# Optimization experiments

Hardware: AMD Instinct MI355X
Metric: run time of the kernel (lower is better)

The kernel has to match this reference:

```python
import jax, jax.numpy as jnp
import numpy as np

N = 100000        # nodes
E = 3200000       # edges (avg degree 32)
B = 64            # graphs in the batch
IN_DIM = 128
HEADS = 4
C1 = 8            # conv1 out_channels per head
C2 = 4            # conv2 out_channels per head
OUT_DIM = 10
EPS = 1e-16       # PyG softmax denominator eps


def _lin(key, fan_in, fan_out):
    return jax.random.normal(key, (fan_in, fan_out), jnp.float32) / np.sqrt(fan_in)


def setup_inputs() -> dict:
    key = jax.random.key(0)
    ks = jax.random.split(key, 16)
    x = jax.random.normal(ks[0], (N, IN_DIM), jnp.float32)
    edge_index = jax.random.randint(ks[1], (2, E), 0, N)
    batch = jnp.sort(jax.random.randint(ks[2], (N,), 0, B))
    d1 = HEADS * C1  # 32
    d2 = HEADS * C2  # 16
    inp = {
        "x": x, "edge_index": edge_index, "batch": batch,
        # conv1 (TransformerConv in=128 -> heads*8 = 32)
        "Wq1": _lin(ks[3], IN_DIM, d1), "bq1": jnp.zeros((d1,), jnp.float32),
        "Wk1": _lin(ks[4], IN_DIM, d1), "bk1": jnp.zeros((d1,), jnp.float32),
        "Wv1": _lin(ks[5], IN_DIM, d1), "bv1": jnp.zeros((d1,), jnp.float32),
        "Ws1": _lin(ks[6], IN_DIM, d1), "bs1": jnp.zeros((d1,), jnp.float32),
        # conv2 (in=32 -> heads*4 = 16)
        "Wq2": _lin(ks[7], d1, d2), "bq2": jnp.zeros((d2,), jnp.float32),
        "Wk2": _lin(ks[8], d1, d2), "bk2": jnp.zeros((d2,), jnp.float32),
        "Wv2": _lin(ks[9], d1, d2), "bv2": jnp.zeros((d2,), jnp.float32),
        "Ws2": _lin(ks[10], d1, d2), "bs2": jnp.zeros((d2,), jnp.float32),
        # fc (16 -> 10)
        "Wfc": _lin(ks[11], d2, OUT_DIM), "bfc": jnp.zeros((OUT_DIM,), jnp.float32),
    }
    return inp


def transformer_conv(x, src, dst, Wq, bq, Wk, bk, Wv, bv, Ws, bs, heads):
    n = x.shape[0]
    hc = Wq.shape[1]
    c = hc // heads
    q = (x @ Wq + bq).reshape(n, heads, c)
    k = (x @ Wk + bk).reshape(n, heads, c)
    v = (x @ Wv + bv).reshape(n, heads, c)
    # edge-wise attention logits: query at dst, key at src -> [E, H]
    alpha = jnp.einsum('ehc,ehc->eh', q[dst], k[src]) / np.sqrt(c).astype(np.float32)
    # segment softmax over incoming edges of each dst node
    amax = jax.ops.segment_max(alpha, dst, num_segments=n)           # [N,H]
    ea = jnp.exp(alpha - amax[dst])
    denom = jax.ops.segment_sum(ea, dst, num_segments=n)             # [N,H]
    w = ea / (denom[dst] + EPS)                                      # [E,H]
    msg = v[src] * w[:, :, None]                                     # [E,H,C]
    out = jax.ops.segment_sum(msg, dst, num_segments=n).reshape(n, hc)
    return out + x @ Ws + bs  # root/skip connection


def reference(x, edge_index, batch,
              Wq1, bq1, Wk1, bk1, Wv1, bv1, Ws1, bs1,
              Wq2, bq2, Wk2, bk2, Wv2, bv2, Ws2, bs2,
              Wfc, bfc):
    src, dst = edge_index[0], edge_index[1]
    h = transformer_conv(x, src, dst, Wq1, bq1, Wk1, bk1, Wv1, bv1, Ws1, bs1, HEADS)
    h = jax.nn.relu(h)
    h = transformer_conv(h, src, dst, Wq2, bq2, Wk2, bk2, Wv2, bv2, Ws2, bs2, HEADS)
    h = jax.nn.relu(h)
    # global mean pool per graph
    sums = jax.ops.segment_sum(h, batch, num_segments=B)             # [B,16]
    cnt = jax.ops.segment_sum(jnp.ones((h.shape[0],), h.dtype), batch, num_segments=B)
    pooled = sums / jnp.maximum(cnt, 1.0)[:, None]
    return pooled @ Wfc + bfc                                        # [B,OUT_DIM]
```

## Files before the change

kernel.cpp:

```cpp
#include <hip/hip_runtime.h>

#define HEADS 4
#define EPS 1e-16f
#define NR 256
#define EPB 2048
#define DCH 2048

typedef float floatx2 __attribute__((ext_vector_type(2)));

__device__ inline int rangeOf(int dst, int rdiv, float rinv) {
    int q = (int)((float)dst * rinv);
    if (q > NR - 1) q = NR - 1;
    if ((long long)q * rdiv > dst) --q;
    else if ((long long)(q + 1) * rdiv <= dst) ++q;
    return q;
}

__global__ __launch_bounds__(256) void scatter_count(
    const int* __restrict__ ei, int E, int rdiv, float rinv,
    int* __restrict__ pcnt)
{
    __shared__ int cnt[NR];
    int b = blockIdx.x, t = threadIdx.x;
    int b0 = b * EPB;
    int nloc = min(EPB, E - b0);
    cnt[t] = 0;
    __syncthreads();
    #pragma unroll
    for (int u = 0; u < 8; ++u) {
        int li = u * 256 + t;
        if (li < nloc)
            atomicAdd(&cnt[rangeOf(ei[E + b0 + li], rdiv, rinv)], 1);
    }
    __syncthreads();
    pcnt[(size_t)b * NR + t] = cnt[t];
}

__global__ __launch_bounds__(256) void qprefix(
    int* __restrict__ pcnt, int nb, int* __restrict__ qtot)
{
    __shared__ int part[256];
    int q = blockIdx.x, t = threadIdx.x;
    int per = (nb + 255) >> 8;
    int lo = t * per, hi = min(lo + per, nb);
    int s = 0;
    for (int b = lo; b < hi; ++b) s += pcnt[(size_t)b * NR + q];
    part[t] = s;
    __syncthreads();
    for (int off = 1; off < 256; off <<= 1) {
        int a = (t >= off) ? part[t - off] : 0;
        __syncthreads();
        part[t] += a;
        __syncthreads();
    }
    if (t == 255) qtot[q] = part[255];
    int pre = (t == 0) ? 0 : part[t - 1];
    for (int b = lo; b < hi; ++b) {
        int c = pcnt[(size_t)b * NR + q];
        pcnt[(size_t)b * NR + q] = pre;
        pre += c;
    }
}

__global__ void qscan(const int* __restrict__ qtot, int* __restrict__ rstart)
{
    __shared__ int tmp[NR];
    int t = threadIdx.x;
    tmp[t] = qtot[t];
    __syncthreads();
    for (int off = 1; off < NR; off <<= 1) {
        int a = (t >= off) ? tmp[t - off] : 0;
        __syncthreads();
        tmp[t] += a;
        __syncthreads();
    }
    rstart[t] = (t == 0) ? 0 : tmp[t - 1];
    if (t == NR - 1) rstart[NR] = tmp[NR - 1];
}

__global__ __launch_bounds__(256) void scatter_place(
    const int* __restrict__ ei, int E, int rdiv, float rinv,
    const int* __restrict__ pcnt, const int* __restrict__ rstart,
    int* __restrict__ rsrc, int* __restrict__ rdst)
{
    __shared__ int2 lrec[EPB];
    __shared__ unsigned char lq[EPB];
    __shared__ int cnt[NR], base[NR], scn[NR];
    int b = blockIdx.x, t = threadIdx.x;
    int b0 = b * EPB;
    int nloc = min(EPB, E - b0);
    cnt[t] = 0;
    __syncthreads();
    int myq[8], myoff[8];
    int2 myrec[8];
    #pragma unroll
    for (int u = 0; u < 8; ++u) {
        int li = u * 256 + t;
        if (li < nloc) {
            int e = b0 + li;
            int sv = ei[e], dv = ei[E + e];
            int q = rangeOf(dv, rdiv, rinv);
            myq[u] = q;
            myrec[u] = make_int2(sv, dv);
            myoff[u] = atomicAdd(&cnt[q], 1);
        } else myq[u] = -1;
    }
    __syncthreads();
    scn[t] = cnt[t];
    __syncthreads();
    for (int off = 1; off < 256; off <<= 1) {
        int a = (t >= off) ? scn[t - off] : 0;
        __syncthreads();
        scn[t] += a;
        __syncthreads();
    }
    base[t] = (t == 0) ? 0 : scn[t - 1];
    __syncthreads();
    #pragma unroll
    for (int u = 0; u < 8; ++u) {
        if (myq[u] >= 0) {
            int slot = base[myq[u]] + myoff[u];
            lrec[slot] = myrec[u];
            lq[slot] = (unsigned char)myq[u];
        }
    }
    __syncthreads();
    #pragma unroll
    for (int u = 0; u < 8; ++u) {
        int s2 = u * 256 + t;
        if (s2 < nloc) {
            int q = lq[s2];
            int g = rstart[q] + pcnt[(size_t)b * NR + q] + (s2 - base[q]);
            int2 r = lrec[s2];
            rsrc[g] = r.x;
            rdst[g] = r.y;
        }
    }
}

__global__ __launch_bounds__(256) void deg_range(
    const int* __restrict__ rdst, const int* __restrict__ rstart,
    int* __restrict__ deg, int* __restrict__ row_ptr, int n, int rdiv, int E)
{
    __shared__ int h[512];
    __shared__ int psum[256];
    int q = blockIdx.x, t = threadIdx.x;
    int lo = q * rdiv, hi = min(lo + rdiv, n);
    int nn = hi - lo;
    if (nn <= 0) {
        if (t == 0 && q == NR - 1) row_ptr[n] = E;
        return;
    }
    for (int i = t; i < 512; i += 256) h[i] = 0;
    __syncthreads();
    int rlo = rstart[q], rhi = rstart[q + 1];
    for (int i = rlo + t; i < rhi; i += 256)
        atomicAdd(&h[rdst[i] - lo], 1);
    __syncthreads();
    int s0 = h[2 * t], s1 = h[2 * t + 1];
    psum[t] = s0 + s1;
    __syncthreads();
    for (int off = 1; off < 256; off <<= 1) {
        int a = (t >= off) ? psum[t - off] : 0;
        __syncthreads();
        psum[t] += a;
        __syncthreads();
    }
    int base = rlo + ((t == 0) ? 0 : psum[t - 1]);
    if (2 * t < nn)     { row_ptr[lo + 2 * t] = base;          deg[lo + 2 * t] = s0; }
    if (2 * t + 1 < nn) { row_ptr[lo + 2 * t + 1] = base + s0; deg[lo + 2 * t + 1] = s1; }
    if (t == 0 && q == NR - 1) row_ptr[n] = E;
}

__global__ __launch_bounds__(256) void place_range(
    const int* __restrict__ rsrc, const int* __restrict__ rdst,
    const int* __restrict__ rstart, const int* __restrict__ row_ptr,
    int* __restrict__ col, int n, int rdiv)
{
    __shared__ int cur[512];
    int q = blockIdx.x;
    int lo = q * rdiv, hi = min(lo + rdiv, n);
    int nn = hi - lo;
    if (nn <= 0) return;
    for (int i = threadIdx.x; i < nn; i += 256) cur[i] = row_ptr[lo + i];
    __syncthreads();
    int rlo = rstart[q], rhi = rstart[q + 1];
    for (int i = rlo + threadIdx.x; i < rhi; i += 256) {
        int pos = atomicAdd(&cur[rdst[i] - lo], 1);
        col[pos] = rsrc[i];
    }
}

__global__ __launch_bounds__(256) void dsort_count(
    const int* __restrict__ deg, int* __restrict__ phd, int n)
{
    __shared__ int h[256];
    int t = threadIdx.x;
    h[t] = 0;
    __syncthreads();
    int lo = blockIdx.x * DCH, hi = min(lo + DCH, n);
    for (int i = lo + t; i < hi; i += 256)
        atomicAdd(&h[min(deg[i], 255)], 1);
    __syncthreads();
    phd[blockIdx.x * 256 + t] = h[t];
}

__global__ __launch_bounds__(256) void dsort_prefix(
    int* __restrict__ phd, int nbd)
{
    __shared__ int tot[256];
    int t = threadIdx.x;
    int s = 0;
    for (int b = 0; b < nbd; ++b) s += phd[b * 256 + t];
    tot[t] = s;
    __syncthreads();
    for (int off = 1; off < 256; off <<= 1) {
        int a = (t >= off) ? tot[t - off] : 0;
        __syncthreads();
        tot[t] += a;
        __syncthreads();
    }
    int running = (t == 0) ? 0 : tot[t - 1];
    for (int b = 0; b < nbd; ++b) {
        int c = phd[b * 256 + t];
        phd[b * 256 + t] = running;
        running += c;
    }
}

__global__ __launch_bounds__(256) void dsort_place(
    const int* __restrict__ deg, const int* __restrict__ phd,
    int* __restrict__ order, int n)
{
    __shared__ int lcur[256];
    int t = threadIdx.x;
    lcur[t] = phd[blockIdx.x * 256 + t];
    __syncthreads();
    int lo = blockIdx.x * DCH, hi = min(lo + DCH, n);
    for (int i = lo + t; i < hi; i += 256) {
        int pos = atomicAdd(&lcur[min(deg[i], 255)], 1);
        order[pos] = i;
    }
}

__global__ __launch_bounds__(256) void proj1_kernel(
    const float* __restrict__ x,
    const float* __restrict__ Wq, const float* __restrict__ bq,
    const float* __restrict__ Wk, const float* __restrict__ bk,
    const float* __restrict__ Wv, const float* __restrict__ bv,
    const float* __restrict__ Ws, const float* __restrict__ bs,
    float* __restrict__ qs1, unsigned char* __restrict__ kv1, int n)
{
    __shared__ float Wl[128][128];
    __shared__ float xl[32][128];
    for (int i = threadIdx.x; i < 128 * 128; i += 256) {
        int k = i >> 7, c = i & 127;
        int sub = c >> 5, j = c & 31;
        const float* W = (sub == 0) ? Wq : (sub == 1) ? Wk : (sub == 2) ? Wv : Ws;
        Wl[k][c] = W[k * 32 + j];
    }
    int col4 = (threadIdx.x & 31) * 4;
    int sub = col4 >> 5, j = col4 & 31;
    float4 bias4;
    {
        const float* b = (sub == 0) ? bq : (sub == 1) ? bk : (sub == 2) ? bv : bs;
        bias4 = *(const float4*)(b + j);
    }
    int rb = (threadIdx.x >> 5) * 4;
    __syncthreads();
    for (int row0 = blockIdx.x * 32; row0 < n; row0 += gridDim.x * 32) {
        #pragma unroll
        for (int u = 0; u < 4; ++u) {
            int i = threadIdx.x + u * 256;
            int r = i >> 5, c4 = (i & 31) * 4;
            int gr = row0 + r;
            float4 xv = (gr < n) ? *(const float4*)(x + (size_t)gr * 128 + c4)
                                 : make_float4(0.f, 0.f, 0.f, 0.f);
            *(float4*)(&xl[r][c4]) = xv;
        }
        __syncthreads();
        float4 a0 = bias4, a1 = bias4, a2 = bias4, a3 = bias4;
        #pragma unroll 4
        for (int k = 0; k < 128; k += 4) {
            float4 xv0 = *(const float4*)(&xl[rb + 0][k]);
            float4 xv1 = *(const float4*)(&xl[rb + 1][k]);
            float4 xv2 = *(const float4*)(&xl[rb + 2][k]);
            float4 xv3 = *(const float4*)(&xl[rb + 3][k]);
            float4 w0 = *(const float4*)(&Wl[k + 0][col4]);
            float4 w1 = *(const float4*)(&Wl[k + 1][col4]);
            float4 w2 = *(const float4*)(&Wl[k + 2][col4]);
            float4 w3 = *(const float4*)(&Wl[k + 3][col4]);
            a0.x += xv0.x*w0.x + xv0.y*w1.x + xv0.z*w2.x + xv0.w*w3.x;
            a0.y += xv0.x*w0.y + xv0.y*w1.y + xv0.z*w2.y + xv0.w*w3.y;
            a0.z += xv0.x*w0.z + xv0.y*w1.z + xv0.z*w2.z + xv0.w*w3.z;
            a0.w += xv0.x*w0.w + xv0.y*w1.w + xv0.z*w2.w + xv0.w*w3.w;
            a1.x += xv1.x*w0.x + xv1.y*w1.x + xv1.z*w2.x + xv1.w*w3.x;
            a1.y += xv1.x*w0.y + xv1.y*w1.y + xv1.z*w2.y + xv1.w*w3.y;
            a1.z += xv1.x*w0.z + xv1.y*w1.z + xv1.z*w2.z + xv1.w*w3.z;
            a1.w += xv1.x*w0.w + xv1.y*w1.w + xv1.z*w2.w + xv1.w*w3.w;
            a2.x += xv2.x*w0.x + xv2.y*w1.x + xv2.z*w2.x + xv2.w*w3.x;
            a2.y += xv2.x*w0.y + xv2.y*w1.y + xv2.z*w2.y + xv2.w*w3.y;
            a2.z += xv2.x*w0.z + xv2.y*w1.z + xv2.z*w2.z + xv2.w*w3.z;
            a2.w += xv2.x*w0.w + xv2.y*w1.w + xv2.z*w2.w + xv2.w*w3.w;
            a3.x += xv3.x*w0.x + xv3.y*w1.x + xv3.z*w2.x + xv3.w*w3.x;
            a3.y += xv3.x*w0.y + xv3.y*w1.y + xv3.z*w2.y + xv3.w*w3.y;
            a3.z += xv3.x*w0.z + xv3.y*w1.z + xv3.z*w2.z + xv3.w*w3.z;
            a3.w += xv3.x*w0.w + xv3.y*w1.w + xv3.z*w2.w + xv3.w*w3.w;
        }
        #pragma unroll
        for (int r = 0; r < 4; ++r) {
            int row = row0 + rb + r;
            if (row < n) {
                float4 acc = (r == 0) ? a0 : (r == 1) ? a1 : (r == 2) ? a2 : a3;
                if (sub == 0)
                    *(float4*)(qs1 + (size_t)row * 64 + j) = acc;
                else if (sub == 3)
                    *(float4*)(qs1 + (size_t)row * 64 + 32 + j) = acc;
                else {
                    unsigned u8 = __builtin_amdgcn_cvt_pk_fp8_f32(acc.x, acc.y, 0u, false);
                    u8 = __builtin_amdgcn_cvt_pk_fp8_f32(acc.z, acc.w, u8, true);
                    *(unsigned*)(kv1 + (size_t)row * 64 + ((sub == 1) ? 0 : 32) + j) = u8;
                }
            }
        }
        __syncthreads();
    }
}

__global__ __launch_bounds__(256) void proj2_kernel(
    const float* __restrict__ h1,
    const float* __restrict__ Wq, const float* __restrict__ bq,
    const float* __restrict__ Wk, const float* __restrict__ bk,
    const float* __restrict__ Wv, const float* __restrict__ bv,
    const float* __restrict__ Ws, const float* __restrict__ bs,
    float* __restrict__ qs2, unsigned char* __restrict__ kv2, int n)
{
    __shared__ float Wl[32][64];
    __shared__ float bl[64];
    __shared__ float xl[4][32];
    for (int i = threadIdx.x; i < 32 * 64; i += 256) {
        int k = i >> 6, c = i & 63;
        int sub = c >> 4, j = c & 15;
        const float* W = (sub == 0) ? Wq : (sub == 1) ? Wk : (sub == 2) ? Wv : Ws;
        Wl[k][c] = W[k * 16 + j];
    }
    if (threadIdx.x < 64) {
        int c = threadIdx.x, sub = c >> 4, j = c & 15;
        const float* b = (sub == 0) ? bq : (sub == 1) ? bk : (sub == 2) ? bv : bs;
        bl[c] = b[j];
    }
    __syncthreads();
    int r = threadIdx.x >> 6, col = threadIdx.x & 63;
    int sub = col >> 4, j = col & 15;
    for (int row0 = blockIdx.x * 4; row0 < n; row0 += gridDim.x * 4) {
        int li = threadIdx.x;
        if (li < 128) {
            int rr = row0 + (li >> 5);
            if (rr < n) xl[li >> 5][li & 31] = h1[(size_t)rr * 32 + (li & 31)];
        }
        __syncthreads();
        int row = row0 + r;
        if (row < n) {
            float acc = bl[col];
            #pragma unroll
            for (int k = 0; k < 32; ++k) acc += xl[r][k] * Wl[k][col];
            if (sub == 0)       qs2[(size_t)row * 32 + j] = acc;
            else if (sub == 3)  qs2[(size_t)row * 32 + 16 + j] = acc;
            else {
                unsigned u8 = __builtin_amdgcn_cvt_pk_fp8_f32(acc, 0.f, 0u, false);
                kv2[(size_t)row * 32 + ((sub == 1) ? 0 : 16) + j] = (unsigned char)(u8 & 0xFF);
            }
        }
        __syncthreads();
    }
}

__global__ __launch_bounds__(256) void gather_conv1(
    const int* __restrict__ row_ptr, const int* __restrict__ order,
    const int* __restrict__ col, const float* __restrict__ qs1,
    const unsigned char* __restrict__ kv1, float* __restrict__ h1, int n)
{
    int tid = blockIdx.x * 256 + threadIdx.x;
    if (tid >= n * HEADS) return;
    int node = order[tid >> 2], h = tid & 3;
    const float4* qp = (const float4*)(qs1 + (size_t)node * 64 + h * 8);
    float4 q0 = qp[0], q1 = qp[1];
    int start = row_ptr[node], d = row_ptr[node + 1] - start;
    float m = -INFINITY, s = 0.f;
    float a0x=0,a0y=0,a0z=0,a0w=0,a1x=0,a1y=0,a1z=0,a1w=0;
    uint2 ku = make_uint2(0,0), vu = make_uint2(0,0);
    if (d > 0) {
        const unsigned char* b0 = kv1 + (size_t)col[start] * 64;
        ku = *(const uint2*)(b0 + h * 8);
        vu = *(const uint2*)(b0 + 32 + h * 8);
    }
    for (int i = 0; i < d; ++i) {
        uint2 kn = ku, vn = vu;
        if (i + 1 < d) {
            const unsigned char* nb = kv1 + (size_t)col[start + i + 1] * 64;
            kn = *(const uint2*)(nb + h * 8);
            vn = *(const uint2*)(nb + 32 + h * 8);
        }
        floatx2 k01 = __builtin_amdgcn_cvt_pk_f32_fp8(ku.x, false);
        floatx2 k23 = __builtin_amdgcn_cvt_pk_f32_fp8(ku.x, true);
        floatx2 k45 = __builtin_amdgcn_cvt_pk_f32_fp8(ku.y, false);
        floatx2 k67 = __builtin_amdgcn_cvt_pk_f32_fp8(ku.y, true);
        float a = (q0.x*k01.x + q0.y*k01.y + q0.z*k23.x + q0.w*k23.y
                 + q1.x*k45.x + q1.y*k45.y + q1.z*k67.x + q1.w*k67.y)
                * 0.35355339059327373f;
        float mn = fmaxf(m, a);
        float corr = __expf(m - mn);
        float ea = __expf(a - mn);
        s = s * corr + ea;
        floatx2 v01 = __builtin_amdgcn_cvt_pk_f32_fp8(vu.x, false);
        floatx2 v23 = __builtin_amdgcn_cvt_pk_f32_fp8(vu.x, true);
        floatx2 v45 = __builtin_amdgcn_cvt_pk_f32_fp8(vu.y, false);
        floatx2 v67 = __builtin_amdgcn_cvt_pk_f32_fp8(vu.y, true);
        a0x = a0x*corr + ea*v01.x; a0y = a0y*corr + ea*v01.y;
        a0z = a0z*corr + ea*v23.x; a0w = a0w*corr + ea*v23.y;
        a1x = a1x*corr + ea*v45.x; a1y = a1y*corr + ea*v45.y;
        a1z = a1z*corr + ea*v67.x; a1w = a1w*corr + ea*v67.y;
        m = mn;
        ku = kn; vu = vn;
    }
    float inv = 1.f / (s + EPS);
    const float* sk = qs1 + (size_t)node * 64 + 32 + h * 8;
    float4 o0, o1;
    o0.x = fmaxf(a0x*inv + sk[0], 0.f); o0.y = fmaxf(a0y*inv + sk[1], 0.f);
    o0.z = fmaxf(a0z*inv + sk[2], 0.f); o0.w = fmaxf(a0w*inv + sk[3], 0.f);
    o1.x = fmaxf(a1x*inv + sk[4], 0.f); o1.y = fmaxf(a1y*inv + sk[5], 0.f);
    o1.z = fmaxf(a1z*inv + sk[6], 0.f); o1.w = fmaxf(a1w*inv + sk[7], 0.f);
    float4* op = (float4*)(h1 + (size_t)node * 32 + h * 8);
    op[0] = o0; op[1] = o1;
}

__global__ __launch_bounds__(256) void gather_conv2(
    const int* __restrict__ row_ptr, const int* __restrict__ order,
    const int* __restrict__ col, const float* __restrict__ qs2,
    const unsigned char* __restrict__ kv2, float* __restrict__ h2, int n)
{
    int tid = blockIdx.x * 256 + threadIdx.x;
    if (tid >= n * HEADS) return;
    int node = order[tid >> 2], h = tid & 3;
    float4 q = *(const float4*)(qs2 + (size_t)node * 32 + h * 4);
    int start = row_ptr[node], d = row_ptr[node + 1] - start;
    float m = -INFINITY, s = 0.f;
    float ax=0, ay=0, az=0, aw=0;
    unsigned ku = 0, vu = 0;
    if (d > 0) {
        const unsigned char* b0 = kv2 + (size_t)col[start] * 32;
        ku = *(const unsigned*)(b0 + h * 4);
        vu = *(const unsigned*)(b0 + 16 + h * 4);
    }
    for (int i = 0; i < d; ++i) {
        unsigned kn = ku, vn = vu;
        if (i + 1 < d) {
            const unsigned char* nb = kv2 + (size_t)col[start + i + 1] * 32;
            kn = *(const unsigned*)(nb + h * 4);
            vn = *(const unsigned*)(nb + 16 + h * 4);
        }
        floatx2 k01 = __builtin_amdgcn_cvt_pk_f32_fp8(ku, false);
        floatx2 k23 = __builtin_amdgcn_cvt_pk_f32_fp8(ku, true);
        float a = (q.x*k01.x + q.y*k01.y + q.z*k23.x + q.w*k23.y) * 0.5f;
        float mn = fmaxf(m, a);
        float corr = __expf(m - mn);
        float ea = __expf(a - mn);
        s = s * corr + ea;
        floatx2 v01 = __builtin_amdgcn_cvt_pk_f32_fp8(vu, false);
        floatx2 v23 = __builtin_amdgcn_cvt_pk_f32_fp8(vu, true);
        ax = ax*corr + ea*v01.x; ay = ay*corr + ea*v01.y;
        az = az*corr + ea*v23.x; aw = aw*corr + ea*v23.y;
        m = mn;
        ku = kn; vu = vn;
    }
    float inv = 1.f / (s + EPS);
    const float* sk = qs2 + (size_t)node * 32 + 16 + h * 4;
    float4 o;
    o.x = fmaxf(ax*inv + sk[0], 0.f);
    o.y = fmaxf(ay*inv + sk[1], 0.f);
    o.z = fmaxf(az*inv + sk[2], 0.f);
    o.w = fmaxf(aw*inv + sk[3], 0.f);
    *(float4*)(h2 + (size_t)node * 16 + h * 4) = o;
}

__global__ __launch_bounds__(256) void pool_kernel(
    const float* __restrict__ h2, const int* __restrict__ batch,
    float* __restrict__ pooled, float* __restrict__ cnt, int n)
{
    __shared__ float acc[16];
    __shared__ int bShared;
    __shared__ int uniform;
    int node0 = blockIdx.x * 16;
    int t = threadIdx.x;
    int node = node0 + (t >> 4), j = t & 15;
    if (t == 0) {
        int bFirst = batch[node0];
        int bLast = batch[min(node0 + 15, n - 1)];
        bShared = bFirst;
        uniform = (bFirst == bLast);
    }
    if (t < 16) acc[t] = 0.f;
    __syncthreads();
    bool active = node < n;
    float val = active ? h2[(size_t)node * 16 + j] : 0.f;
    if (uniform) {
        if (active) atomicAdd(&acc[j], val);
        __syncthreads();
        int nlocal = min(16, n - node0);
        if (t < 16) atomicAdd(pooled + bShared * 16 + t, acc[t]);
        if (t == 0) atomicAdd(cnt + bShared, (float)nlocal);
    } else {
        if (active) {
            int b = batch[node];
            atomicAdd(pooled + b * 16 + j, val);
            if (j == 0) atomicAdd(cnt + b, 1.f);
        }
    }
}

__global__ void fc_kernel(
    const float* __restrict__ pooled, const float* __restrict__ cnt,
    const float* __restrict__ Wfc, const float* __restrict__ bfc,
    float* __restrict__ out)
{
    int t = threadIdx.x;
    if (t < 64 * 10) {
        int b = t / 10, o = t % 10;
        float c = fmaxf(cnt[b], 1.0f);
        float acc = bfc[o];
        #pragma unroll
        for (int k = 0; k < 16; ++k)
            acc += (pooled[b * 16 + k] / c) * Wfc[k * 10 + o];
        out[t] = acc;
    }
}

extern "C" void kernel_launch(void* const* d_in, const int* in_sizes, int n_in,
                              void* d_out, int out_size, void* d_ws, size_t ws_size,
                              hipStream_t stream) {
    const float* x     = (const float*)d_in[0];
    const int*   ei    = (const int*)d_in[1];
    const int*   batch = (const int*)d_in[2];
    const float* Wq1 = (const float*)d_in[3],  *bq1 = (const float*)d_in[4];
    const float* Wk1 = (const float*)d_in[5],  *bk1 = (const float*)d_in[6];
    const float* Wv1 = (const float*)d_in[7],  *bv1 = (const float*)d_in[8];
    const float* Ws1 = (const float*)d_in[9],  *bs1 = (const float*)d_in[10];
    const float* Wq2 = (const float*)d_in[11], *bq2 = (const float*)d_in[12];
    const float* Wk2 = (const float*)d_in[13], *bk2 = (const float*)d_in[14];
    const float* Wv2 = (const float*)d_in[15], *bv2 = (const float*)d_in[16];
    const float* Ws2 = (const float*)d_in[17], *bs2 = (const float*)d_in[18];
    const float* Wfc = (const float*)d_in[19], *bfc = (const float*)d_in[20];

    int N = in_sizes[0] / 128;
    int E = in_sizes[1] / 2;
    int rdiv = (N + NR - 1) / NR;
    float rinv = 1.0f / (float)rdiv;
    int NB = (E + EPB - 1) / EPB;
    int NBD = (N + DCH - 1) / DCH;

    float* ws = (float*)d_ws;
    float* qs1    = ws;
    float* h1     = qs1 + (size_t)N * 64;
    float* h2     = h1 + (size_t)N * 32;
    float* qs2    = h2 + (size_t)N * 16;
    float* pooled = qs2 + (size_t)N * 32;
    float* cnt    = pooled + 1024;
    unsigned char* kv1 = (unsigned char*)(cnt + 64);
    unsigned char* kv2 = kv1 + (size_t)N * 64;
    int* deg     = (int*)(kv2 + (size_t)N * 32);
    int* row_ptr = deg + N;
    int* rstart  = row_ptr + N + 1;
    int* qtot    = rstart + NR + 1;
    int* col     = qtot + NR;
    int* order   = col + E;
    int* pcnt    = order + N;
    int* phd     = pcnt + (size_t)NB * NR;
    int* rsrc = (int*)h1;
    int* rdst = (int*)h2;

    hipMemsetAsync(pooled, 0, (1024 + 64) * sizeof(float), stream);

    int ngrid = (N * HEADS + 255) / 256;

    scatter_count<<<NB, 256, 0, stream>>>(ei, E, rdiv, rinv, pcnt);
    qprefix<<<NR, 256, 0, stream>>>(pcnt, NB, qtot);
    qscan<<<1, NR, 0, stream>>>(qtot, rstart);
    scatter_place<<<NB, 256, 0, stream>>>(ei, E, rdiv, rinv, pcnt, rstart, rsrc, rdst);
    deg_range<<<NR, 256, 0, stream>>>(rdst, rstart, deg, row_ptr, N, rdiv, E);
    place_range<<<NR, 256, 0, stream>>>(rsrc, rdst, rstart, row_ptr, col, N, rdiv);

    dsort_count<<<NBD, 256, 0, stream>>>(deg, phd, N);
    dsort_prefix<<<1, 256, 0, stream>>>(phd, NBD);
    dsort_place<<<NBD, 256, 0, stream>>>(deg, phd, order, N);

    proj1_kernel<<<1024, 256, 0, stream>>>(x, Wq1, bq1, Wk1, bk1, Wv1, bv1, Ws1, bs1, qs1, kv1, N);
    gather_conv1<<<ngrid, 256, 0, stream>>>(row_ptr, order, col, qs1, kv1, h1, N);

    proj2_kernel<<<1024, 256, 0, stream>>>(h1, Wq2, bq2, Wk2, bk2, Wv2, bv2, Ws2, bs2, qs2, kv2, N);
    gather_conv2<<<ngrid, 256, 0, stream>>>(row_ptr, order, col, qs2, kv2, h2, N);

    pool_kernel<<<(N + 15) / 16, 256, 0, stream>>>(h2, batch, pooled, cnt, N);
    fc_kernel<<<1, 640, 0, stream>>>(pooled, cnt, Wfc, bfc, (float*)d_out);
}
```

Baseline: 386.1 us.

## Fuse degree-sort histogram into CSR build and split proj1 columns across blocks

```diff
diff --git a/kernel.cpp b/kernel.cpp
--- a/kernel.cpp
+++ b/kernel.cpp
@@ -4,7 +4,6 @@
 #define EPS 1e-16f
 #define NR 256
 #define EPB 2048
-#define DCH 2048
 
 typedef float floatx2 __attribute__((ext_vector_type(2)));
 
@@ -140,18 +139,21 @@
 
 __global__ __launch_bounds__(256) void deg_range(
     const int* __restrict__ rdst, const int* __restrict__ rstart,
-    int* __restrict__ deg, int* __restrict__ row_ptr, int n, int rdiv, int E)
+    int* __restrict__ deg, int* __restrict__ row_ptr,
+    int* __restrict__ phd, int n, int rdiv, int E)
 {
     __shared__ int h[512];
     __shared__ int psum[256];
+    __shared__ int hd[256];
     int q = blockIdx.x, t = threadIdx.x;
     int lo = q * rdiv, hi = min(lo + rdiv, n);
     int nn = hi - lo;
     if (nn <= 0) {
+        phd[q * 256 + t] = 0;
         if (t == 0 && q == NR - 1) row_ptr[n] = E;
         return;
     }
-    for (int i = t; i < 512; i += 256) h[i] = 0;
+    h[t] = 0; h[t + 256] = 0; hd[t] = 0;
     __syncthreads();
     int rlo = rstart[q], rhi = rstart[q + 1];
     for (int i = rlo + t; i < rhi; i += 256)
@@ -167,42 +169,19 @@
         __syncthreads();
     }
     int base = rlo + ((t == 0) ? 0 : psum[t - 1]);
-    if (2 * t < nn)     { row_ptr[lo + 2 * t] = base;          deg[lo + 2 * t] = s0; }
-    if (2 * t + 1 < nn) { row_ptr[lo + 2 * t + 1] = base + s0; deg[lo + 2 * t + 1] = s1; }
+    if (2 * t < nn) {
+        row_ptr[lo + 2 * t] = base;
+        deg[lo + 2 * t] = s0;
+        atomicAdd(&hd[min(s0, 255)], 1);
+    }
+    if (2 * t + 1 < nn) {
+        row_ptr[lo + 2 * t + 1] = base + s0;
+        deg[lo + 2 * t + 1] = s1;
+        atomicAdd(&hd[min(s1, 255)], 1);
+    }
     if (t == 0 && q == NR - 1) row_ptr[n] = E;
-}
-
-__global__ __launch_bounds__(256) void place_range(
-    const int* __restrict__ rsrc, const int* __restrict__ rdst,
-    const int* __restrict__ rstart, const int* __restrict__ row_ptr,
-    int* __restrict__ col, int n, int rdiv)
-{
-    __shared__ int cur[512];
-    int q = blockIdx.x;
-    int lo = q * rdiv, hi = min(lo + rdiv, n);
-    int nn = hi - lo;
-    if (nn <= 0) return;
-    for (int i = threadIdx.x; i < nn; i += 256) cur[i] = row_ptr[lo + i];
-    __syncthreads();
-    int rlo = rstart[q], rhi = rstart[q + 1];
-    for (int i = rlo + threadIdx.x; i < rhi; i += 256) {
-        int pos = atomicAdd(&cur[rdst[i] - lo], 1);
-        col[pos] = rsrc[i];
-    }
-}
-
-__global__ __launch_bounds__(256) void dsort_count(
-    const int* __restrict__ deg, int* __restrict__ phd, int n)
-{
-    __shared__ int h[256];
-    int t = threadIdx.x;
-    h[t] = 0;
-    __syncthreads();
-    int lo = blockIdx.x * DCH, hi = min(lo + DCH, n);
-    for (int i = lo + t; i < hi; i += 256)
-        atomicAdd(&h[min(deg[i], 255)], 1);
-    __syncthreads();
-    phd[blockIdx.x * 256 + t] = h[t];
+    __syncthreads();
+    phd[q * 256 + t] = hd[t];
 }
 
 __global__ __launch_bounds__(256) void dsort_prefix(
@@ -228,18 +207,29 @@
     }
 }
 
-__global__ __launch_bounds__(256) void dsort_place(
+__global__ __launch_bounds__(256) void place_range(
+    const int* __restrict__ rsrc, const int* __restrict__ rdst,
+    const int* __restrict__ rstart, const int* __restrict__ row_ptr,
     const int* __restrict__ deg, const int* __restrict__ phd,
-    int* __restrict__ order, int n)
-{
+    int* __restrict__ col, int* __restrict__ order, int n, int rdiv)
+{
+    __shared__ int cur[512];
     __shared__ int lcur[256];
-    int t = threadIdx.x;
-    lcur[t] = phd[blockIdx.x * 256 + t];
-    __syncthreads();
-    int lo = blockIdx.x * DCH, hi = min(lo + DCH, n);
-    for (int i = lo + t; i < hi; i += 256) {
-        int pos = atomicAdd(&lcur[min(deg[i], 255)], 1);
-        order[pos] = i;
+    int q = blockIdx.x, t = threadIdx.x;
+    int lo = q * rdiv, hi = min(lo + rdiv, n);
+    int nn = hi - lo;
+    if (nn <= 0) return;
+    for (int i = t; i < nn; i += 256) cur[i] = row_ptr[lo + i];
+    lcur[t] = phd[q * 256 + t];
+    __syncthreads();
+    int rlo = rstart[q], rhi = rstart[q + 1];
+    for (int i = rlo + t; i < rhi; i += 256) {
+        int pos = atomicAdd(&cur[rdst[i] - lo], 1);
+        col[pos] = rsrc[i];
+    }
+    for (int i = t; i < nn; i += 256) {
+        int pos = atomicAdd(&lcur[min(deg[lo + i], 255)], 1);
+        order[pos] = lo + i;
     }
 }
 
@@ -251,24 +241,28 @@
     const float* __restrict__ Ws, const float* __restrict__ bs,
     float* __restrict__ qs1, unsigned char* __restrict__ kv1, int n)
 {
-    __shared__ float Wl[128][128];
+    __shared__ float Wl[128][64];
     __shared__ float xl[32][128];
-    for (int i = threadIdx.x; i < 128 * 128; i += 256) {
-        int k = i >> 7, c = i & 127;
-        int sub = c >> 5, j = c & 31;
+    int half = blockIdx.x & 1;
+    for (int i = threadIdx.x; i < 128 * 64; i += 256) {
+        int k = i >> 6, c = i & 63;
+        int gc = half * 64 + c;
+        int sub = gc >> 5, j = gc & 31;
         const float* W = (sub == 0) ? Wq : (sub == 1) ? Wk : (sub == 2) ? Wv : Ws;
         Wl[k][c] = W[k * 32 + j];
     }
-    int col4 = (threadIdx.x & 31) * 4;
-    int sub = col4 >> 5, j = col4 & 31;
+    int col4 = (threadIdx.x & 15) * 4;
+    int gcol4 = half * 64 + col4;
+    int sub = gcol4 >> 5, j = gcol4 & 31;
     float4 bias4;
     {
         const float* b = (sub == 0) ? bq : (sub == 1) ? bk : (sub == 2) ? bv : bs;
         bias4 = *(const float4*)(b + j);
     }
-    int rb = (threadIdx.x >> 5) * 4;
-    __syncthreads();
-    for (int row0 = blockIdx.x * 32; row0 < n; row0 += gridDim.x * 32) {
+    int rb = (threadIdx.x >> 4) * 2;
+    __syncthreads();
+    int rstride = (gridDim.x >> 1) * 32;
+    for (int row0 = (blockIdx.x >> 1) * 32; row0 < n; row0 += rstride) {
         #pragma unroll
         for (int u = 0; u < 4; ++u) {
             int i = threadIdx.x + u * 256;
@@ -279,39 +273,19 @@
             *(float4*)(&xl[r][c4]) = xv;
         }
         __syncthreads();
-        float4 a0 = bias4, a1 = bias4, a2 = bias4, a3 = bias4;
-        #pragma unroll 4
-        for (int k = 0; k < 128; k += 4) {
-            float4 xv0 = *(const float4*)(&xl[rb + 0][k]);
-            float4 xv1 = *(const float4*)(&xl[rb + 1][k]);
-            float4 xv2 = *(const float4*)(&xl[rb + 2][k]);
-            float4 xv3 = *(const float4*)(&xl[rb + 3][k]);
-            float4 w0 = *(const float4*)(&Wl[k + 0][col4]);
-            float4 w1 = *(const float4*)(&Wl[k + 1][col4]);
-            float4 w2 = *(const float4*)(&Wl[k + 2][col4]);
-            float4 w3 = *(const float4*)(&Wl[k + 3][col4]);
-            a0.x += xv0.x*w0.x + xv0.y*w1.x + xv0.z*w2.x + xv0.w*w3.x;
-            a0.y += xv0.x*w0.y + xv0.y*w1.y + xv0.z*w2.y + xv0.w*w3.y;
-            a0.z += xv0.x*w0.z + xv0.y*w1.z + xv0.z*w2.z + xv0.w*w3.z;
-            a0.w += xv0.x*w0.w + xv0.y*w1.w + xv0.z*w2.w + xv0.w*w3.w;
-            a1.x += xv1.x*w0.x + xv1.y*w1.x + xv1.z*w2.x + xv1.w*w3.x;
-            a1.y += xv1.x*w0.y + xv1.y*w1.y + xv1.z*w2.y + xv1.w*w3.y;
-            a1.z += xv1.x*w0.z + xv1.y*w1.z + xv1.z*w2.z + xv1.w*w3.z;
-            a1.w += xv1.x*w0.w + xv1.y*w1.w + xv1.z*w2.w + xv1.w*w3.w;
-            a2.x += xv2.x*w0.x + xv2.y*w1.x + xv2.z*w2.x + xv2.w*w3.x;
-            a2.y += xv2.x*w0.y + xv2.y*w1.y + xv2.z*w2.y + xv2.w*w3.y;
-            a2.z += xv2.x*w0.z + xv2.y*w1.z + xv2.z*w2.z + xv2.w*w3.z;
-            a2.w += xv2.x*w0.w + xv2.y*w1.w + xv2.z*w2.w + xv2.w*w3.w;
-            a3.x += xv3.x*w0.x + xv3.y*w1.x + xv3.z*w2.x + xv3.w*w3.x;
-            a3.y += xv3.x*w0.y + xv3.y*w1.y + xv3.z*w2.y + xv3.w*w3.y;
-            a3.z += xv3.x*w0.z + xv3.y*w1.z + xv3.z*w2.z + xv3.w*w3.z;
-            a3.w += xv3.x*w0.w + xv3.y*w1.w + xv3.z*w2.w + xv3.w*w3.w;
+        float4 a0 = bias4, a1 = bias4;
+        #pragma unroll 8
+        for (int k = 0; k < 128; ++k) {
+            float4 w = *(const float4*)(&Wl[k][col4]);
+            float x0 = xl[rb + 0][k], x1 = xl[rb + 1][k];
+            a0.x += x0 * w.x; a0.y += x0 * w.y; a0.z += x0 * w.z; a0.w += x0 * w.w;
+            a1.x += x1 * w.x; a1.y += x1 * w.y; a1.z += x1 * w.z; a1.w += x1 * w.w;
         }
         #pragma unroll
-        for (int r = 0; r < 4; ++r) {
+        for (int r = 0; r < 2; ++r) {
             int row = row0 + rb + r;
             if (row < n) {
-                float4 acc = (r == 0) ? a0 : (r == 1) ? a1 : (r == 2) ? a2 : a3;
+                float4 acc = (r == 0) ? a0 : a1;
                 if (sub == 0)
                     *(float4*)(qs1 + (size_t)row * 64 + j) = acc;
                 else if (sub == 3)
@@ -556,7 +530,6 @@
     int rdiv = (N + NR - 1) / NR;
     float rinv = 1.0f / (float)rdiv;
     int NB = (E + EPB - 1) / EPB;
-    int NBD = (N + DCH - 1) / DCH;
 
     float* ws = (float*)d_ws;
     float* qs1    = ws;
@@ -586,14 +559,11 @@
     qprefix<<<NR, 256, 0, stream>>>(pcnt, NB, qtot);
     qscan<<<1, NR, 0, stream>>>(qtot, rstart);
     scatter_place<<<NB, 256, 0, stream>>>(ei, E, rdiv, rinv, pcnt, rstart, rsrc, rdst);
-    deg_range<<<NR, 256, 0, stream>>>(rdst, rstart, deg, row_ptr, N, rdiv, E);
-    place_range<<<NR, 256, 0, stream>>>(rsrc, rdst, rstart, row_ptr, col, N, rdiv);
-
-    dsort_count<<<NBD, 256, 0, stream>>>(deg, phd, N);
-    dsort_prefix<<<1, 256, 0, stream>>>(phd, NBD);
-    dsort_place<<<NBD, 256, 0, stream>>>(deg, phd, order, N);
-
-    proj1_kernel<<<1024, 256, 0, stream>>>(x, Wq1, bq1, Wk1, bk1, Wv1, bv1, Ws1, bs1, qs1, kv1, N);
+    deg_range<<<NR, 256, 0, stream>>>(rdst, rstart, deg, row_ptr, phd, N, rdiv, E);
+    dsort_prefix<<<1, 256, 0, stream>>>(phd, NR);
+    place_range<<<NR, 256, 0, stream>>>(rsrc, rdst, rstart, row_ptr, deg, phd, col, order, N, rdiv);
+
+    proj1_kernel<<<2048, 256, 0, stream>>>(x, Wq1, bq1, Wk1, bk1, Wv1, bv1, Ws1, bs1, qs1, kv1, N);
     gather_conv1<<<ngrid, 256, 0, stream>>>(row_ptr, order, col, qs1, kv1, h1, N);
 
     proj2_kernel<<<1024, 256, 0, stream>>>(h1, Wq2, bq2, Wk2, bk2, Wv2, bv2, Ws2, bs2, qs2, kv2, N);
```

New measurement: 428.4 us. 1.11x slower.
